# Kernel tuning notes

Hardware: AMD Instinct MI355X
Metric: run time of the kernel (lower is better)

## Reference

```python
import jax, jax.numpy as jnp
import numpy as np
from jax import lax

K = 8          # num_classes
C_IN = 256     # in_channels
EPS = 1e-5


def resize_bilinear_ac(x, H, W):
    """Bilinear resize with align_corners=True. x: [B,C,h,w] -> [B,C,H,W]."""
    B, C, h, w = x.shape
    if h == H and w == W:
        return x
    ys = jnp.linspace(0.0, h - 1.0, H)
    xs = jnp.linspace(0.0, w - 1.0, W)
    y0 = jnp.floor(ys).astype(jnp.int32)
    x0 = jnp.floor(xs).astype(jnp.int32)
    y1 = jnp.minimum(y0 + 1, h - 1)
    x1 = jnp.minimum(x0 + 1, w - 1)
    wy = (ys - y0.astype(x.dtype))[None, None, :, None]
    wx = (xs - x0.astype(x.dtype))[None, None, None, :]
    g00 = x[:, :, y0][:, :, :, x0]
    g01 = x[:, :, y0][:, :, :, x1]
    g10 = x[:, :, y1][:, :, :, x0]
    g11 = x[:, :, y1][:, :, :, x1]
    top = g00 * (1.0 - wx) + g01 * wx
    bot = g10 * (1.0 - wx) + g11 * wx
    return top * (1.0 - wy) + bot * wy


def setup_inputs() -> dict:
    key = jax.random.key(0)
    ks = jax.random.split(key, 16)
    shapes = [(2, 256, 128, 128), (2, 256, 64, 64), (2, 256, 32, 32), (2, 256, 16, 16), (2, 256, 8, 8)]
    inp = {}
    for i, s in enumerate(shapes):
        inp[f"feat{i}"] = jax.random.normal(ks[i], s, dtype=jnp.float32)
    inp["attr_feat"] = jax.random.normal(ks[5], (2, K * C_IN, 64, 64), dtype=jnp.float32)
    # learned params
    inp["mlp_f_w"] = jax.random.normal(ks[6], (256, 256), dtype=jnp.float32) * 0.02
    inp["mlp_f_b"] = jnp.zeros((256,), dtype=jnp.float32)
    inp["mlp_a_w"] = jax.random.normal(ks[7], (256, 256), dtype=jnp.float32) * 0.02
    inp["mlp_a_b"] = jnp.zeros((256,), dtype=jnp.float32)
    # 5 grouped convs: [out=2048, in_per_group=256, 3, 3] each, no bias (BN follows)
    inp["conv_w"] = jax.random.normal(ks[8], (5, K * C_IN, C_IN, 3, 3), dtype=jnp.float32) * 0.02
    inp["bn_gamma"] = jnp.ones((5, K * C_IN), dtype=jnp.float32)
    inp["bn_beta"] = jnp.zeros((5, K * C_IN), dtype=jnp.float32)
    inp["bn_mean"] = jax.random.normal(ks[9], (5, K * C_IN), dtype=jnp.float32) * 0.1
    inp["bn_var"] = jax.random.uniform(ks[10], (5, K * C_IN), dtype=jnp.float32, minval=0.5, maxval=1.5)
    return inp


def _forward(feats, attr_feat, mlp_f_w, mlp_f_b, mlp_a_w, mlp_a_b, conv_w, bn_gamma, bn_beta, bn_mean, bn_var):
    B = attr_feat.shape[0]
    # global avg pool attr -> [B, K, C] -> mlp_a
    avg_attr = attr_feat.mean(axis=(2, 3)).reshape(B, K, C_IN)
    avg_attr = avg_attr @ mlp_a_w.T + mlp_a_b  # [B,K,256]
    outs = []
    for i, x in enumerate(feats):
        _, C, H, W = x.shape
        avg_x = x.mean(axis=(2, 3)) @ mlp_f_w.T + mlp_f_b          # [B,256]
        logits = jnp.einsum('bkc,bc->bk', avg_attr, avg_x)          # [B,K]
        attn = jax.nn.softmax(logits, axis=-1)
        y = resize_bilinear_ac(attr_feat, H, W)                      # [B,2048,H,W]
        y = lax.conv_general_dilated(
            y, conv_w[i], window_strides=(1, 1), padding=((1, 1), (1, 1)),
            dimension_numbers=('NCHW', 'OIHW', 'NCHW'), feature_group_count=K)
        inv = lax.rsqrt(bn_var[i] + EPS)
        y = (y - bn_mean[i][None, :, None, None]) * (inv * bn_gamma[i])[None, :, None, None] + bn_beta[i][None, :, None, None]
        y = jax.nn.relu(y)
        y = y.reshape(B, K, C, H, W)
        y = jnp.einsum('bkchw,bk->bchw', y, attn)                   # weighted sum over classes
        outs.append(jax.nn.relu(x + y))
    return tuple(outs)


def reference(feat0, feat1, feat2, feat3, feat4, attr_feat, mlp_f_w, mlp_f_b, mlp_a_w, mlp_a_b, conv_w, bn_gamma, bn_beta, bn_mean, bn_var):
    feats = [feat0, feat1, feat2, feat3, feat4]
    return _forward(feats, attr_feat, mlp_f_w, mlp_f_b, mlp_a_w, mlp_a_b, conv_w, bn_gamma, bn_beta, bn_mean, bn_var)
```

## Files before the change

### kernel.cpp

```cpp
#include <hip/hip_runtime.h>
#include <hip/hip_bf16.h>
#include <cstdint>

typedef __attribute__((ext_vector_type(8))) short short8;
typedef __attribute__((ext_vector_type(4))) float f32x4;

#define EPSV 1e-5f

__device__ __forceinline__ void gload_lds16(const void* g, void* l) {
  __builtin_amdgcn_global_load_lds(
      (const __attribute__((address_space(1))) void*)(uintptr_t)g,
      (__attribute__((address_space(3))) void*)(uint32_t)(uintptr_t)l,
      16, 0, 0);
}

__global__ void mean_kernel(const float* __restrict__ in, float* __restrict__ out,
                            int HW, float inv) {
  const int ch = blockIdx.x;
  const int t = threadIdx.x;
  const float* p = in + (size_t)ch * HW;
  float s = 0.f;
  const int nv = HW >> 2;
  const float4* pv = (const float4*)p;
  for (int i = t; i < nv; i += 256) { float4 v = pv[i]; s += v.x + v.y + v.z + v.w; }
  __shared__ float red[256];
  red[t] = s; __syncthreads();
  for (int off = 128; off > 0; off >>= 1) {
    if (t < off) red[t] += red[t + off];
    __syncthreads();
  }
  if (t == 0) out[ch] = red[0] * inv;
}

__global__ void wtrans_kernel(const float* __restrict__ cw,
                              const float* __restrict__ gamma, const float* __restrict__ beta,
                              const float* __restrict__ mean, const float* __restrict__ var,
                              __hip_bfloat16* __restrict__ wt, float* __restrict__ bias) {
  const int oc = blockIdx.x;
  const int i  = blockIdx.y;
  const int ci = threadIdx.x;
  const int idx = i * 2048 + oc;
  const float sc = rsqrtf(var[idx] + EPSV) * gamma[idx];
  if (ci == 0) bias[idx] = beta[idx] - mean[idx] * sc;
  const int g = oc >> 8, co = oc & 255;
  const float* src = cw + ((size_t)idx * 256 + ci) * 9;
  const size_t dbase = (size_t)(i * 8 + g) * 9 * 65536 + co * 256 + ci;
#pragma unroll
  for (int tap = 0; tap < 9; ++tap)
    wt[dbase + (size_t)tap * 65536] = __float2bfloat16(src[tap] * sc);
}

__global__ void gate_kernel(const float* __restrict__ meanA, const float* __restrict__ meanF,
                            const float* __restrict__ Wa, const float* __restrict__ ba,
                            const float* __restrict__ Wf, const float* __restrict__ bfp,
                            float* __restrict__ attn) {
  __shared__ float mA[16 * 256];
  __shared__ float mF[10 * 256];
  __shared__ float pA[16 * 256];
  __shared__ float pF[10 * 256];
  __shared__ float lg[80];
  const int t = threadIdx.x;
  for (int i = t; i < 4096; i += 256) mA[i] = meanA[i];
  for (int i = t; i < 2560; i += 256) mF[i] = meanF[i];
  __syncthreads();
  {
    float acc[16];
#pragma unroll
    for (int j = 0; j < 16; ++j) acc[j] = 0.f;
    for (int ci = 0; ci < 256; ++ci) {
      const float w = Wa[t * 256 + ci];
#pragma unroll
      for (int j = 0; j < 16; ++j) acc[j] += mA[j * 256 + ci] * w;
    }
    const float bb = ba[t];
#pragma unroll
    for (int j = 0; j < 16; ++j) pA[j * 256 + t] = acc[j] + bb;
  }
  {
    float acc[10];
#pragma unroll
    for (int j = 0; j < 10; ++j) acc[j] = 0.f;
    for (int ci = 0; ci < 256; ++ci) {
      const float w = Wf[t * 256 + ci];
#pragma unroll
      for (int j = 0; j < 10; ++j) acc[j] += mF[j * 256 + ci] * w;
    }
    const float bb = bfp[t];
#pragma unroll
    for (int j = 0; j < 10; ++j) pF[j * 256 + t] = acc[j] + bb;
  }
  __syncthreads();
  if (t < 80) {
    const int i = t >> 4, r = t & 15, b = r >> 3, k = r & 7;
    const float* a = &pA[(b * 8 + k) * 256];
    const float* f = &pF[(i * 2 + b) * 256];
    float d = 0.f;
    for (int c = 0; c < 256; ++c) d += a[c] * f[c];
    lg[t] = d;
  }
  __syncthreads();
  if (t < 10) {
    const int base = t * 8;
    float m = lg[base];
    for (int k = 1; k < 8; ++k) m = fmaxf(m, lg[base + k]);
    float e[8], s = 0.f;
    for (int k = 0; k < 8; ++k) { e[k] = __expf(lg[base + k] - m); s += e[k]; }
    const float invs = 1.f / s;
    for (int k = 0; k < 8; ++k) attn[base + k] = e[k] * invs;
  }
}

__global__ void resize_kernel(const float* __restrict__ attr,
                              __hip_bfloat16* __restrict__ R,
                              int W, int Hp, int Wp, float scl) {
  const int bk = blockIdx.x;
  const int yp = blockIdx.y;
  const int t  = threadIdx.x;
  const size_t rowbase = ((size_t)bk * Hp + yp) * (size_t)Wp * 256;
  if (yp == 0 || yp == Hp - 1) {
    uint32_t* p = (uint32_t*)(R + rowbase);
    const int n = Wp * 128;
    for (int idx = t; idx < n; idx += 256) p[idx] = 0u;
    return;
  }
  const int y = yp - 1;
  const float fy = y * scl;
  int y0 = (int)floorf(fy); if (y0 > 63) y0 = 63;
  const float wy = fy - (float)y0;
  const int y1 = min(y0 + 1, 63);
  __shared__ float buf[2][64][65];
  const int cc = t >> 2, seg = (t & 3) * 16;
  const int bb = bk >> 3, k = bk & 7;
  const float* ab = attr + (size_t)bb * 2048 * 4096;
  const int ci = t & 63;
  for (int cq = 0; cq < 4; ++cq) {
    __syncthreads();
    {
      const int ch = k * 256 + cq * 64 + cc;
      const float* r0 = ab + ((size_t)ch * 64 + y0) * 64;
      const float* r1 = ab + ((size_t)ch * 64 + y1) * 64;
#pragma unroll
      for (int u = 0; u < 4; ++u) {
        float4 v0 = ((const float4*)r0)[(t & 3) * 4 + u];
        float4 v1 = ((const float4*)r1)[(t & 3) * 4 + u];
        buf[0][cc][seg + u * 4 + 0] = v0.x; buf[0][cc][seg + u * 4 + 1] = v0.y;
        buf[0][cc][seg + u * 4 + 2] = v0.z; buf[0][cc][seg + u * 4 + 3] = v0.w;
        buf[1][cc][seg + u * 4 + 0] = v1.x; buf[1][cc][seg + u * 4 + 1] = v1.y;
        buf[1][cc][seg + u * 4 + 2] = v1.z; buf[1][cc][seg + u * 4 + 3] = v1.w;
      }
    }
    __syncthreads();
    for (int x = t >> 6; x < W; x += 4) {
      const float fx = x * scl;
      int x0 = (int)floorf(fx); if (x0 > 63) x0 = 63;
      const float wx = fx - (float)x0;
      const int x1 = min(x0 + 1, 63);
      const float top = buf[0][ci][x0] * (1.f - wx) + buf[0][ci][x1] * wx;
      const float bot = buf[1][ci][x0] * (1.f - wx) + buf[1][ci][x1] * wx;
      R[rowbase + (size_t)(x + 1) * 256 + cq * 64 + ci] = __float2bfloat16(top * (1.f - wy) + bot * wy);
    }
    if (t < 64) {
      R[rowbase + cq * 64 + t] = __float2bfloat16(0.f);
      R[rowbase + (size_t)(Wp - 1) * 256 + cq * 64 + t] = __float2bfloat16(0.f);
    }
  }
}

__global__ __launch_bounds__(256, 2)
void conv_kernel(const __hip_bfloat16* __restrict__ R,
                 const __hip_bfloat16* __restrict__ Wt,
                 const float* __restrict__ bias,
                 const float* __restrict__ attn,
                 const float* __restrict__ featp,
                 float* __restrict__ outp,
                 int W, int lw, int Hp, int Wp, int HW,
                 int b0, int NB, int gcount) {
  __shared__ alignas(16) __hip_bfloat16 ldsA[2][128 * 64];
  __shared__ alignas(16) __hip_bfloat16 ldsB[2][128 * 64];
  const int tid  = threadIdx.x;
  const int lane = tid & 63;
  const int wave = __builtin_amdgcn_readfirstlane(tid >> 6);
  const int wm = (wave >> 1) * 64;
  const int wn = (wave & 1) * 64;
  const int co0 = blockIdx.y * 128;
  const int n0  = blockIdx.x * 128;
  const int bb  = (int)blockIdx.z % NB;
  const int gs  = (int)blockIdx.z / NB;
  const int b   = b0 + bb;
  const int g0  = gs * gcount;

  const int c8 = lane & 7;
  const int r8 = lane >> 3;
  int aoff[4], boff[4];
#pragma unroll
  for (int q = 0; q < 4; ++q) {
    const int row = (wave * 4 + q) * 8 + r8;
    const int sc = (c8 ^ (row & 7)) << 3;
    aoff[q] = ((co0 + row) << 8) + sc;
    int sg = n0 + row; if (sg >= HW) sg = HW - 1;
    const int y = sg >> lw, x = sg & (W - 1);
    boff[q] = (y * Wp + x) * 256 + sc;
  }

  const size_t rgstride = (size_t)Hp * Wp * 256;
  const __hip_bfloat16* Rb = R + (size_t)bb * 8 * rgstride;

  const f32x4 fz = {0.f, 0.f, 0.f, 0.f};
  f32x4 fin[4][4], acc[4][4];
#pragma unroll
  for (int mf = 0; mf < 4; ++mf)
#pragma unroll
    for (int nf = 0; nf < 4; ++nf) { fin[mf][nf] = fz; acc[mf][nf] = fz; }

  {
    const __hip_bfloat16* wp = Wt + ((size_t)g0 * 9 << 16);
    const __hip_bfloat16* rp = Rb + (size_t)g0 * rgstride;
#pragma unroll
    for (int q = 0; q < 4; ++q) {
      gload_lds16(wp + aoff[q], &ldsA[0][(wave * 4 + q) * 512]);
      gload_lds16(rp + boff[q], &ldsB[0][(wave * 4 + q) * 512]);
    }
  }
  int cqp = 0, txp = 0, typ = 0, gp = g0;
  int foldc = 0, gcur = g0;
  const int nstages = gcount * 36;

  for (int s = 0; s < nstages; ++s) {
    __builtin_amdgcn_s_barrier();
    asm volatile("" ::: "memory");
    if (s + 1 < nstages) {
      ++cqp;
      if (cqp == 4) {
        cqp = 0; ++txp;
        if (txp == 3) { txp = 0; ++typ; if (typ == 3) { typ = 0; ++gp; } }
      }
      const __hip_bfloat16* wp = Wt + (((size_t)gp * 9 + typ * 3 + txp) << 16) + (cqp << 6);
      const __hip_bfloat16* rp = Rb + (size_t)gp * rgstride + ((typ * Wp + txp) << 8) + (cqp << 6);
      const int nb = (s + 1) & 1;
#pragma unroll
      for (int q = 0; q < 4; ++q) {
        gload_lds16(wp + aoff[q], &ldsA[nb][(wave * 4 + q) * 512]);
        gload_lds16(rp + boff[q], &ldsB[nb][(wave * 4 + q) * 512]);
      }
      asm volatile("s_waitcnt vmcnt(8)" ::: "memory");
    } else {
      asm volatile("s_waitcnt vmcnt(0)" ::: "memory");
    }
    __builtin_amdgcn_s_barrier();
    asm volatile("" ::: "memory");

    const int cb0 = s & 1;
#pragma unroll
    for (int ks = 0; ks < 2; ++ks) {
      short8 af[4], bfv[4];
      const int cb = ks * 4 + (lane >> 4);
#pragma unroll
      for (int mf = 0; mf < 4; ++mf) {
        const int row = wm + mf * 16 + (lane & 15);
        af[mf] = *(const short8*)&ldsA[cb0][(row << 6) + ((cb ^ (row & 7)) << 3)];
      }
#pragma unroll
      for (int nf = 0; nf < 4; ++nf) {
        const int row = wn + nf * 16 + (lane & 15);
        bfv[nf] = *(const short8*)&ldsB[cb0][(row << 6) + ((cb ^ (row & 7)) << 3)];
      }
#pragma unroll
      for (int mf = 0; mf < 4; ++mf)
#pragma unroll
        for (int nf = 0; nf < 4; ++nf)
          acc[mf][nf] = __builtin_amdgcn_mfma_f32_16x16x32_bf16(
              af[mf], bfv[nf], acc[mf][nf], 0, 0, 0);
    }

    if (++foldc == 36) {
      foldc = 0;
      const float aw = attn[b * 8 + gcur];
#pragma unroll
      for (int mf = 0; mf < 4; ++mf) {
        const int cobase = co0 + wm + mf * 16 + ((lane >> 4) << 2);
#pragma unroll
        for (int r = 0; r < 4; ++r) {
          const float bs = bias[(gcur << 8) + cobase + r];
#pragma unroll
          for (int nf = 0; nf < 4; ++nf) {
            fin[mf][nf][r] += aw * fmaxf(acc[mf][nf][r] + bs, 0.f);
            acc[mf][nf][r] = 0.f;
          }
        }
      }
      ++gcur;
    }
  }

  const size_t plane = (size_t)256 * HW;
  if (featp) {
    const float* fb = featp + (size_t)b * plane;
    float* ob = outp + (size_t)b * plane;
#pragma unroll
    for (int mf = 0; mf < 4; ++mf) {
      const int cobase = co0 + wm + mf * 16 + ((lane >> 4) << 2);
#pragma unroll
      for (int nf = 0; nf < 4; ++nf) {
        const int n = n0 + wn + nf * 16 + (lane & 15);
        if (n < HW) {
#pragma unroll
          for (int r = 0; r < 4; ++r) {
            const size_t idx = (size_t)(cobase + r) * HW + n;
            ob[idx] = fmaxf(fb[idx] + fin[mf][nf][r], 0.f);
          }
        }
      }
    }
  } else {
    float* zb = outp + ((size_t)gs * 2 + b) * plane;
#pragma unroll
    for (int mf = 0; mf < 4; ++mf) {
      const int cobase = co0 + wm + mf * 16 + ((lane >> 4) << 2);
#pragma unroll
      for (int nf = 0; nf < 4; ++nf) {
        const int n = n0 + wn + nf * 16 + (lane & 15);
        if (n < HW) {
#pragma unroll
          for (int r = 0; r < 4; ++r)
            zb[(size_t)(cobase + r) * HW + n] = fin[mf][nf][r];
        }
      }
    }
  }
}

__global__ void reduce_kernel(const float* __restrict__ z, const float* __restrict__ feat,
                              float* __restrict__ outp, int total, int S) {
  const int idx = blockIdx.x * 256 + threadIdx.x;
  if (idx >= total) return;
  float s = feat[idx];
  for (int j = 0; j < S; ++j) s += z[(size_t)j * total + idx];
  outp[idx] = fmaxf(s, 0.f);
}

extern "C" void kernel_launch(void* const* d_in, const int* in_sizes, int n_in,
                              void* d_out, int out_size, void* d_ws, size_t ws_size,
                              hipStream_t stream) {
  const float* feat[5];
  for (int i = 0; i < 5; ++i) feat[i] = (const float*)d_in[i];
  const float* attr = (const float*)d_in[5];
  const float* mfw = (const float*)d_in[6];
  const float* mfb = (const float*)d_in[7];
  const float* maw = (const float*)d_in[8];
  const float* mab = (const float*)d_in[9];
  const float* cw  = (const float*)d_in[10];
  const float* bng = (const float*)d_in[11];
  const float* bnb = (const float*)d_in[12];
  const float* bnm = (const float*)d_in[13];
  const float* bnv = (const float*)d_in[14];
  float* out = (float*)d_out;

  char* ws = (char*)d_ws;
  float* attnW = (float*)(ws);
  float* meanA = (float*)(ws + 512);
  float* meanF = (float*)(ws + 20480);
  float* biasW = (float*)(ws + 32768);
  __hip_bfloat16* Wt = (__hip_bfloat16*)(ws + 131072);
  const size_t R_OFF = 47316992;
  __hip_bfloat16* Rbuf = (__hip_bfloat16*)(ws + R_OFF);

  const bool full = ws_size >= (size_t)219316224;
  const int NB = full ? 2 : 1;
  float* zbuf = (float*)(ws + R_OFF + (size_t)NB * 69222400);

  static const int HS[5] = {128, 64, 32, 16, 8};
  static const size_t OOFF[5] = {0, 8388608, 10485760, 11010048, 11141120};
  static const int SPLIT[5] = {1, 4, 8, 8, 8};

  mean_kernel<<<4096, 256, 0, stream>>>(attr, meanA, 4096, 1.f / 4096.f);
  for (int i = 0; i < 5; ++i) {
    const int HW = HS[i] * HS[i];
    mean_kernel<<<512, 256, 0, stream>>>(feat[i], meanF + i * 512, HW, 1.f / (float)HW);
  }
  wtrans_kernel<<<dim3(2048, 5), 256, 0, stream>>>(cw, bng, bnb, bnm, bnv, Wt, biasW);
  gate_kernel<<<1, 256, 0, stream>>>(meanA, meanF, maw, mab, mfw, mfb, attnW);

  for (int i = 0; i < 5; ++i) {
    const int H = HS[i], W = H, HW = H * W, Hp = H + 2, Wp = W + 2;
    const int lw = 31 - __builtin_clz((unsigned)W);
    const float scl = 63.f / (float)(H - 1);
    const int S = full ? SPLIT[i] : 1;
    const int gcount = 8 / S;
    for (int b0 = 0; b0 < 2; b0 += NB) {
      resize_kernel<<<dim3(NB * 8, Hp), 256, 0, stream>>>(
          attr + (size_t)b0 * 2048 * 4096, Rbuf, W, Hp, Wp, scl);
      const float* fp = (S == 1) ? feat[i] : nullptr;
      float* op = (S == 1) ? (out + OOFF[i]) : zbuf;
      conv_kernel<<<dim3((HW + 127) / 128, 2, NB * S), 256, 0, stream>>>(
          Rbuf, Wt + (size_t)i * 8 * 9 * 65536, biasW + i * 2048, attnW + i * 16,
          fp, op, W, lw, Hp, Wp, HW, b0, NB, gcount);
    }
    if (S > 1) {
      const int total = 2 * 256 * HW;
      reduce_kernel<<<(total + 255) / 256, 256, 0, stream>>>(zbuf, feat[i], out + OOFF[i], total, S);
    }
  }
}
```

Before: 751.0 us.

## Widen conv tile to all 256 output channels and triple-buffer LDS loads

```diff
diff --git a/kernel.cpp b/kernel.cpp
--- a/kernel.cpp
+++ b/kernel.cpp
@@ -166,7 +166,20 @@
   }
 }
 
-__global__ __launch_bounds__(256, 2)
+__device__ __forceinline__ void issue_stage(
+    const __hip_bfloat16* __restrict__ Wt, const __hip_bfloat16* __restrict__ Rb,
+    size_t rgstride, int gp, int typ, int txp, int cqp, int Wp,
+    const int* aoff, const int* adst, const int* boff, const int* bdst,
+    __hip_bfloat16* bufA, __hip_bfloat16* bufB) {
+  const __hip_bfloat16* wp = Wt + (((size_t)gp * 9 + typ * 3 + txp) << 16) + (cqp << 6);
+  const __hip_bfloat16* rp = Rb + (size_t)gp * rgstride + ((typ * Wp + txp) << 8) + (cqp << 6);
+#pragma unroll
+  for (int q = 0; q < 4; ++q) gload_lds16(wp + aoff[q], bufA + adst[q]);
+#pragma unroll
+  for (int q = 0; q < 2; ++q) gload_lds16(rp + boff[q], bufB + bdst[q]);
+}
+
+__global__ __launch_bounds__(512, 2)
 void conv_kernel(const __hip_bfloat16* __restrict__ R,
                  const __hip_bfloat16* __restrict__ Wt,
                  const float* __restrict__ bias,
@@ -175,31 +188,35 @@
                  float* __restrict__ outp,
                  int W, int lw, int Hp, int Wp, int HW,
                  int b0, int NB, int gcount) {
-  __shared__ alignas(16) __hip_bfloat16 ldsA[2][128 * 64];
-  __shared__ alignas(16) __hip_bfloat16 ldsB[2][128 * 64];
+  __shared__ alignas(16) __hip_bfloat16 ldsA[3][256 * 64];
+  __shared__ alignas(16) __hip_bfloat16 ldsB[3][128 * 64];
   const int tid  = threadIdx.x;
   const int lane = tid & 63;
   const int wave = __builtin_amdgcn_readfirstlane(tid >> 6);
   const int wm = (wave >> 1) * 64;
   const int wn = (wave & 1) * 64;
-  const int co0 = blockIdx.y * 128;
   const int n0  = blockIdx.x * 128;
-  const int bb  = (int)blockIdx.z % NB;
-  const int gs  = (int)blockIdx.z / NB;
+  const int bb  = (int)blockIdx.y % NB;
+  const int gs  = (int)blockIdx.y / NB;
   const int b   = b0 + bb;
   const int g0  = gs * gcount;
 
   const int c8 = lane & 7;
   const int r8 = lane >> 3;
-  int aoff[4], boff[4];
+  int aoff[4], adst[4], boff[2], bdst[2];
 #pragma unroll
   for (int q = 0; q < 4; ++q) {
-    const int row = (wave * 4 + q) * 8 + r8;
-    const int sc = (c8 ^ (row & 7)) << 3;
-    aoff[q] = ((co0 + row) << 8) + sc;
+    const int row = wave * 32 + q * 8 + r8;
+    aoff[q] = (row << 8) + ((c8 ^ (row & 7)) << 3);
+    adst[q] = (wave * 32 + q * 8) << 6;
+  }
+#pragma unroll
+  for (int q = 0; q < 2; ++q) {
+    const int row = wave * 16 + q * 8 + r8;
     int sg = n0 + row; if (sg >= HW) sg = HW - 1;
     const int y = sg >> lw, x = sg & (W - 1);
-    boff[q] = (y * Wp + x) * 256 + sc;
+    boff[q] = ((y * Wp + x) << 8) + ((c8 ^ (row & 7)) << 3);
+    bdst[q] = (wave * 16 + q * 8) << 6;
   }
 
   const size_t rgstride = (size_t)Hp * Wp * 256;
@@ -212,44 +229,37 @@
 #pragma unroll
     for (int nf = 0; nf < 4; ++nf) { fin[mf][nf] = fz; acc[mf][nf] = fz; }
 
-  {
-    const __hip_bfloat16* wp = Wt + ((size_t)g0 * 9 << 16);
-    const __hip_bfloat16* rp = Rb + (size_t)g0 * rgstride;
-#pragma unroll
-    for (int q = 0; q < 4; ++q) {
-      gload_lds16(wp + aoff[q], &ldsA[0][(wave * 4 + q) * 512]);
-      gload_lds16(rp + boff[q], &ldsB[0][(wave * 4 + q) * 512]);
-    }
-  }
-  int cqp = 0, txp = 0, typ = 0, gp = g0;
+  issue_stage(Wt, Rb, rgstride, g0, 0, 0, 0, Wp, aoff, adst, boff, bdst,
+              &ldsA[0][0], &ldsB[0][0]);
+  issue_stage(Wt, Rb, rgstride, g0, 0, 0, 1, Wp, aoff, adst, boff, bdst,
+              &ldsA[1][0], &ldsB[1][0]);
+  int cqp = 1, txp = 0, typ = 0, gp = g0;
+  int cur = 0, nbf = 2;
   int foldc = 0, gcur = g0;
   const int nstages = gcount * 36;
 
   for (int s = 0; s < nstages; ++s) {
     __builtin_amdgcn_s_barrier();
     asm volatile("" ::: "memory");
-    if (s + 1 < nstages) {
+    if (s + 2 < nstages) {
       ++cqp;
       if (cqp == 4) {
         cqp = 0; ++txp;
         if (txp == 3) { txp = 0; ++typ; if (typ == 3) { typ = 0; ++gp; } }
       }
-      const __hip_bfloat16* wp = Wt + (((size_t)gp * 9 + typ * 3 + txp) << 16) + (cqp << 6);
-      const __hip_bfloat16* rp = Rb + (size_t)gp * rgstride + ((typ * Wp + txp) << 8) + (cqp << 6);
-      const int nb = (s + 1) & 1;
-#pragma unroll
-      for (int q = 0; q < 4; ++q) {
-        gload_lds16(wp + aoff[q], &ldsA[nb][(wave * 4 + q) * 512]);
-        gload_lds16(rp + boff[q], &ldsB[nb][(wave * 4 + q) * 512]);
-      }
-      asm volatile("s_waitcnt vmcnt(8)" ::: "memory");
+      issue_stage(Wt, Rb, rgstride, gp, typ, txp, cqp, Wp, aoff, adst, boff, bdst,
+                  &ldsA[nbf][0], &ldsB[nbf][0]);
+      asm volatile("s_waitcnt vmcnt(12)" ::: "memory");
+    } else if (s + 1 < nstages) {
+      asm volatile("s_waitcnt vmcnt(6)" ::: "memory");
     } else {
       asm volatile("s_waitcnt vmcnt(0)" ::: "memory");
     }
     __builtin_amdgcn_s_barrier();
     asm volatile("" ::: "memory");
 
-    const int cb0 = s & 1;
+    const __hip_bfloat16* pA = &ldsA[cur][0];
+    const __hip_bfloat16* pB = &ldsB[cur][0];
 #pragma unroll
     for (int ks = 0; ks < 2; ++ks) {
       short8 af[4], bfv[4];
@@ -257,12 +267,12 @@
 #pragma unroll
       for (int mf = 0; mf < 4; ++mf) {
         const int row = wm + mf * 16 + (lane & 15);
-        af[mf] = *(const short8*)&ldsA[cb0][(row << 6) + ((cb ^ (row & 7)) << 3)];
+        af[mf] = *(const short8*)&pA[(row << 6) + ((cb ^ (row & 7)) << 3)];
       }
 #pragma unroll
       for (int nf = 0; nf < 4; ++nf) {
         const int row = wn + nf * 16 + (lane & 15);
-        bfv[nf] = *(const short8*)&ldsB[cb0][(row << 6) + ((cb ^ (row & 7)) << 3)];
+        bfv[nf] = *(const short8*)&pB[(row << 6) + ((cb ^ (row & 7)) << 3)];
       }
 #pragma unroll
       for (int mf = 0; mf < 4; ++mf)
@@ -272,12 +282,15 @@
               af[mf], bfv[nf], acc[mf][nf], 0, 0, 0);
     }
 
+    if (++cur == 3) cur = 0;
+    if (++nbf == 3) nbf = 0;
+
     if (++foldc == 36) {
       foldc = 0;
       const float aw = attn[b * 8 + gcur];
 #pragma unroll
       for (int mf = 0; mf < 4; ++mf) {
-        const int cobase = co0 + wm + mf * 16 + ((lane >> 4) << 2);
+        const int cobase = wm + mf * 16 + ((lane >> 4) << 2);
 #pragma unroll
         for (int r = 0; r < 4; ++r) {
           const float bs = bias[(gcur << 8) + cobase + r];
@@ -298,7 +311,7 @@
     float* ob = outp + (size_t)b * plane;
 #pragma unroll
     for (int mf = 0; mf < 4; ++mf) {
-      const int cobase = co0 + wm + mf * 16 + ((lane >> 4) << 2);
+      const int cobase = wm + mf * 16 + ((lane >> 4) << 2);
 #pragma unroll
       for (int nf = 0; nf < 4; ++nf) {
         const int n = n0 + wn + nf * 16 + (lane & 15);
@@ -315,7 +328,7 @@
     float* zb = outp + ((size_t)gs * 2 + b) * plane;
 #pragma unroll
     for (int mf = 0; mf < 4; ++mf) {
-      const int cobase = co0 + wm + mf * 16 + ((lane >> 4) << 2);
+      const int cobase = wm + mf * 16 + ((lane >> 4) << 2);
 #pragma unroll
       for (int nf = 0; nf < 4; ++nf) {
         const int n = n0 + wn + nf * 16 + (lane & 15);
@@ -391,7 +404,7 @@
           attr + (size_t)b0 * 2048 * 4096, Rbuf, W, Hp, Wp, scl);
       const float* fp = (S == 1) ? feat[i] : nullptr;
       float* op = (S == 1) ? (out + OOFF[i]) : zbuf;
-      conv_kernel<<<dim3((HW + 127) / 128, 2, NB * S), 256, 0, stream>>>(
+      conv_kernel<<<dim3((HW + 127) / 128, NB * S), 512, 0, stream>>>(
           Rbuf, Wt + (size_t)i * 8 * 9 * 65536, biasW + i * 2048, attnW + i * 16,
           fp, op, W, lw, Hp, Wp, HW, b0, NB, gcount);
     }
```

Result: slower. 822.7 us (+9.5%).

## Triple-buffer activation tiles with two-stage prefetch and remap block indices for locality

Applied to the files above, without the earlier changes.

```diff
diff --git a/kernel.cpp b/kernel.cpp
--- a/kernel.cpp
+++ b/kernel.cpp
@@ -166,6 +166,15 @@
   }
 }
 
+__device__ __forceinline__ void coords36(int u, int g0, int& g, int& ty, int& tx, int& cq) {
+  g = g0 + u / 36;
+  const int r = u % 36;
+  const int tap = r >> 2;
+  cq = r & 3;
+  ty = tap / 3;
+  tx = tap - ty * 3;
+}
+
 __global__ __launch_bounds__(256, 2)
 void conv_kernel(const __hip_bfloat16* __restrict__ R,
                  const __hip_bfloat16* __restrict__ Wt,
@@ -176,22 +185,27 @@
                  int W, int lw, int Hp, int Wp, int HW,
                  int b0, int NB, int gcount) {
   __shared__ alignas(16) __hip_bfloat16 ldsA[2][128 * 64];
-  __shared__ alignas(16) __hip_bfloat16 ldsB[2][128 * 64];
+  __shared__ alignas(16) __hip_bfloat16 ldsB[3][128 * 64];
   const int tid  = threadIdx.x;
   const int lane = tid & 63;
   const int wave = __builtin_amdgcn_readfirstlane(tid >> 6);
   const int wm = (wave >> 1) * 64;
   const int wn = (wave & 1) * 64;
-  const int co0 = blockIdx.y * 128;
-  const int n0  = blockIdx.x * 128;
-  const int bb  = (int)blockIdx.z % NB;
-  const int gs  = (int)blockIdx.z / NB;
+
+  const int nx  = gridDim.x;
+  const int lin = blockIdx.x;
+  const int pos = ((nx & 7) == 0) ? ((lin & 7) * (nx >> 3) + (lin >> 3)) : lin;
+  const int co0 = (pos & 1) * 128;
+  const int n0  = (pos >> 1) * 128;
+
+  const int bb  = (int)blockIdx.y % NB;
+  const int gs  = (int)blockIdx.y / NB;
   const int b   = b0 + bb;
   const int g0  = gs * gcount;
 
   const int c8 = lane & 7;
   const int r8 = lane >> 3;
-  int aoff[4], boff[4];
+  int aoff[4], boff[4], dst[4];
 #pragma unroll
   for (int q = 0; q < 4; ++q) {
     const int row = (wave * 4 + q) * 8 + r8;
@@ -199,7 +213,8 @@
     aoff[q] = ((co0 + row) << 8) + sc;
     int sg = n0 + row; if (sg >= HW) sg = HW - 1;
     const int y = sg >> lw, x = sg & (W - 1);
-    boff[q] = (y * Wp + x) * 256 + sc;
+    boff[q] = ((y * Wp + x) << 8) + sc;
+    dst[q] = (wave * 4 + q) * 512;
   }
 
   const size_t rgstride = (size_t)Hp * Wp * 256;
@@ -212,44 +227,53 @@
 #pragma unroll
     for (int nf = 0; nf < 4; ++nf) { fin[mf][nf] = fz; acc[mf][nf] = fz; }
 
+  const int nstages = gcount * 36;
+
   {
-    const __hip_bfloat16* wp = Wt + ((size_t)g0 * 9 << 16);
-    const __hip_bfloat16* rp = Rb + (size_t)g0 * rgstride;
-#pragma unroll
-    for (int q = 0; q < 4; ++q) {
-      gload_lds16(wp + aoff[q], &ldsA[0][(wave * 4 + q) * 512]);
-      gload_lds16(rp + boff[q], &ldsB[0][(wave * 4 + q) * 512]);
-    }
-  }
-  int cqp = 0, txp = 0, typ = 0, gp = g0;
+    int g, ty, tx, cq;
+    coords36(0, g0, g, ty, tx, cq);
+    const __hip_bfloat16* wp = Wt + (((size_t)g * 9 + ty * 3 + tx) << 16) + (cq << 6);
+    const __hip_bfloat16* rp = Rb + (size_t)g * rgstride + ((ty * Wp + tx) << 8) + (cq << 6);
+#pragma unroll
+    for (int q = 0; q < 4; ++q) gload_lds16(wp + aoff[q], &ldsA[0][dst[q]]);
+#pragma unroll
+    for (int q = 0; q < 4; ++q) gload_lds16(rp + boff[q], &ldsB[0][dst[q]]);
+    coords36(1, g0, g, ty, tx, cq);
+    const __hip_bfloat16* rp1 = Rb + (size_t)g * rgstride + ((ty * Wp + tx) << 8) + (cq << 6);
+#pragma unroll
+    for (int q = 0; q < 4; ++q) gload_lds16(rp1 + boff[q], &ldsB[1][dst[q]]);
+  }
+
+  int bcur = 0, b2 = 2;
   int foldc = 0, gcur = g0;
-  const int nstages = gcount * 36;
 
   for (int s = 0; s < nstages; ++s) {
     __builtin_amdgcn_s_barrier();
     asm volatile("" ::: "memory");
     if (s + 1 < nstages) {
-      ++cqp;
-      if (cqp == 4) {
-        cqp = 0; ++txp;
-        if (txp == 3) { txp = 0; ++typ; if (typ == 3) { typ = 0; ++gp; } }
-      }
-      const __hip_bfloat16* wp = Wt + (((size_t)gp * 9 + typ * 3 + txp) << 16) + (cqp << 6);
-      const __hip_bfloat16* rp = Rb + (size_t)gp * rgstride + ((typ * Wp + txp) << 8) + (cqp << 6);
-      const int nb = (s + 1) & 1;
-#pragma unroll
-      for (int q = 0; q < 4; ++q) {
-        gload_lds16(wp + aoff[q], &ldsA[nb][(wave * 4 + q) * 512]);
-        gload_lds16(rp + boff[q], &ldsB[nb][(wave * 4 + q) * 512]);
-      }
-      asm volatile("s_waitcnt vmcnt(8)" ::: "memory");
-    } else {
-      asm volatile("s_waitcnt vmcnt(0)" ::: "memory");
-    }
+      int g, ty, tx, cq;
+      coords36(s + 1, g0, g, ty, tx, cq);
+      const __hip_bfloat16* wp = Wt + (((size_t)g * 9 + ty * 3 + tx) << 16) + (cq << 6);
+      __hip_bfloat16* dA = &ldsA[(s + 1) & 1][0];
+#pragma unroll
+      for (int q = 0; q < 4; ++q) gload_lds16(wp + aoff[q], dA + dst[q]);
+    }
+    if (s + 2 < nstages) {
+      int g, ty, tx, cq;
+      coords36(s + 2, g0, g, ty, tx, cq);
+      const __hip_bfloat16* rp = Rb + (size_t)g * rgstride + ((ty * Wp + tx) << 8) + (cq << 6);
+      __hip_bfloat16* dB = &ldsB[b2][0];
+#pragma unroll
+      for (int q = 0; q < 4; ++q) gload_lds16(rp + boff[q], dB + dst[q]);
+    }
+    if (s + 2 < nstages)      asm volatile("s_waitcnt vmcnt(12)" ::: "memory");
+    else if (s + 1 < nstages) asm volatile("s_waitcnt vmcnt(8)" ::: "memory");
+    else                      asm volatile("s_waitcnt vmcnt(0)" ::: "memory");
     __builtin_amdgcn_s_barrier();
     asm volatile("" ::: "memory");
 
-    const int cb0 = s & 1;
+    const __hip_bfloat16* pA = &ldsA[s & 1][0];
+    const __hip_bfloat16* pB = &ldsB[bcur][0];
 #pragma unroll
     for (int ks = 0; ks < 2; ++ks) {
       short8 af[4], bfv[4];
@@ -257,12 +281,12 @@
 #pragma unroll
       for (int mf = 0; mf < 4; ++mf) {
         const int row = wm + mf * 16 + (lane & 15);
-        af[mf] = *(const short8*)&ldsA[cb0][(row << 6) + ((cb ^ (row & 7)) << 3)];
+        af[mf] = *(const short8*)&pA[(row << 6) + ((cb ^ (row & 7)) << 3)];
       }
 #pragma unroll
       for (int nf = 0; nf < 4; ++nf) {
         const int row = wn + nf * 16 + (lane & 15);
-        bfv[nf] = *(const short8*)&ldsB[cb0][(row << 6) + ((cb ^ (row & 7)) << 3)];
+        bfv[nf] = *(const short8*)&pB[(row << 6) + ((cb ^ (row & 7)) << 3)];
       }
 #pragma unroll
       for (int mf = 0; mf < 4; ++mf)
@@ -271,6 +295,9 @@
           acc[mf][nf] = __builtin_amdgcn_mfma_f32_16x16x32_bf16(
               af[mf], bfv[nf], acc[mf][nf], 0, 0, 0);
     }
+
+    if (++bcur == 3) bcur = 0;
+    if (++b2 == 3) b2 = 0;
 
     if (++foldc == 36) {
       foldc = 0;
@@ -386,12 +413,13 @@
     const float scl = 63.f / (float)(H - 1);
     const int S = full ? SPLIT[i] : 1;
     const int gcount = 8 / S;
+    const int ntiles = (HW + 127) / 128;
     for (int b0 = 0; b0 < 2; b0 += NB) {
       resize_kernel<<<dim3(NB * 8, Hp), 256, 0, stream>>>(
           attr + (size_t)b0 * 2048 * 4096, Rbuf, W, Hp, Wp, scl);
       const float* fp = (S == 1) ? feat[i] : nullptr;
       float* op = (S == 1) ? (out + OOFF[i]) : zbuf;
-      conv_kernel<<<dim3((HW + 127) / 128, 2, NB * S), 256, 0, stream>>>(
+      conv_kernel<<<dim3(ntiles * 2, NB * S), 256, 0, stream>>>(
           Rbuf, Wt + (size_t)i * 8 * 9 * 65536, biasW + i * 2048, attnW + i * 16,
           fp, op, W, lw, Hp, Wp, HW, b0, NB, gcount);
     }
```

Result: no change. 742.6 us (-1.1%).
